# Performance work log

Measured on AMD Instinct MI355X. Metric: run time of the kernel, lower is better.

The kernel has to match this reference:

```python
import jax, jax.numpy as jnp
import numpy as np

N = 100000
E = 3200000
IN_C = 256
HID = 64
OUT_C = 2
EPS = 1e-5


def setup_inputs() -> dict:
    key = jax.random.key(0)
    ks = jax.random.split(key, 8)
    x = jax.random.normal(ks[0], (N, IN_C), dtype=jnp.float32)
    edge_index = jax.random.randint(ks[1], (2, E), 0, N, dtype=jnp.int64)
    # GCNConv weights (PyG: out = A_hat @ (x W) + b)
    W1 = jax.random.normal(ks[2], (IN_C, HID), dtype=jnp.float32) / np.sqrt(IN_C)
    b1 = jnp.zeros((HID,), dtype=jnp.float32)
    W2 = jax.random.normal(ks[3], (HID, OUT_C), dtype=jnp.float32) / np.sqrt(HID)
    b2 = jnp.zeros((OUT_C,), dtype=jnp.float32)
    # BatchNorm affine params
    g1 = jnp.ones((HID,), dtype=jnp.float32)
    be1 = jnp.zeros((HID,), dtype=jnp.float32)
    g2 = jnp.ones((OUT_C,), dtype=jnp.float32)
    be2 = jnp.zeros((OUT_C,), dtype=jnp.float32)
    # Decoder linear
    Wd = jax.random.normal(ks[4], (OUT_C, IN_C), dtype=jnp.float32) / np.sqrt(OUT_C)
    bd = jnp.zeros((IN_C,), dtype=jnp.float32)
    return {"x": x, "edge_index": edge_index, "W1": W1, "b1": b1, "g1": g1,
            "be1": be1, "W2": W2, "b2": b2, "g2": g2, "be2": be2,
            "Wd": Wd, "bd": bd}


def gcn_conv(x, W, b, src, dst, n):
    # x: [N, Cin] -> [N, Cout]; symmetric-normalized aggregation with self-loops
    xw = x @ W  # [N, Cout]
    loops = jnp.arange(n, dtype=src.dtype)
    s = jnp.concatenate([src, loops])  # [E+N]
    d = jnp.concatenate([dst, loops])
    deg = jax.ops.segment_sum(jnp.ones_like(d, dtype=x.dtype), d, num_segments=n)
    dinv = jax.lax.rsqrt(deg)  # deg >= 1 thanks to self-loops
    norm = dinv[s] * dinv[d]   # [E+N]
    out = jax.ops.segment_sum(norm[:, None] * xw[s], d, num_segments=n)
    return out + b


def batch_norm(x, gamma, beta):
    # training-mode BN over node dim, biased variance (torch semantics)
    mu = jnp.mean(x, axis=0)
    var = jnp.mean(jnp.square(x - mu), axis=0)
    return (x - mu) * jax.lax.rsqrt(var + EPS) * gamma + beta


def reference(x, edge_index, W1, b1, g1, be1, W2, b2, g2, be2, Wd, bd):
    src, dst = edge_index[0], edge_index[1]
    n = x.shape[0]
    h = gcn_conv(x, W1, b1, src, dst, n)
    h = jax.nn.relu(batch_norm(h, g1, be1))
    # dropout: identity (inference)
    z = batch_norm(gcn_conv(h, W2, b2, src, dst, n), g2, be2)
    return z @ Wd + bd  # decoder: [N, IN_C]
```

## Files before the change

### kernel.cpp

```cpp
#include <hip/hip_runtime.h>
#include <hip/hip_bf16.h>

#define NN 100000
#define NE 3200000
#define INC 256
#define HID 64
#define OUTC 2
#define EPSV 1e-5f

#define NBUCK 128
#define BCAP  26000
#define BIN_CHUNK 4096
#define BIN_K 16
#define BIN_GRID ((NE + BIN_CHUNK - 1) / BIN_CHUNK)

#define NQUART 25000

typedef short short8 __attribute__((ext_vector_type(8)));
typedef float f32x4 __attribute__((ext_vector_type(4)));

static __device__ __forceinline__ float bf2f(unsigned short u) {
    return __uint_as_float((unsigned)u << 16);
}
static __device__ __forceinline__ unsigned short f2bf(float f) {
    __hip_bfloat16 hb = __float2bfloat16(f);
    return *(unsigned short*)&hb;
}

__global__ __launch_bounds__(256) void bin_kernel(const int* __restrict__ src,
                                                  const int* __restrict__ dst,
                                                  int* __restrict__ gtail,
                                                  unsigned int* __restrict__ pbuf) {
    __shared__ int bcnt[NBUCK], bbase[NBUCK];
    int t = threadIdx.x;
    if (t < NBUCK) bcnt[t] = 0;
    __syncthreads();
    int base = blockIdx.x * BIN_CHUNK;
    int s[BIN_K], d[BIN_K], sl[BIN_K], bk[BIN_K];
#pragma unroll
    for (int r = 0; r < BIN_K; r++) {
        int i = base + r * 256 + t;
        bool v = i < NE;
        s[r] = v ? src[i] : 0;
        d[r] = v ? dst[i] : 0;
        bk[r] = (int)(((unsigned)d[r] * (unsigned)NBUCK) / (unsigned)NN);
        sl[r] = v ? atomicAdd(&bcnt[bk[r]], 1) : 0;
    }
    __syncthreads();
    if (t < NBUCK) bbase[t] = bcnt[t] ? atomicAdd(&gtail[t], bcnt[t]) : 0;
    __syncthreads();
#pragma unroll
    for (int r = 0; r < BIN_K; r++) {
        int i = base + r * 256 + t;
        if (i < NE) {
            int b = bk[r];
            int nbase = (b * NN + NBUCK - 1) >> 7;
            pbuf[(size_t)b * BCAP + bbase[b] + sl[r]] =
                ((unsigned)(d[r] - nbase) << 17) | (unsigned)s[r];
        }
    }
}

__global__ void bscan_kernel(const int* __restrict__ gtail, int* __restrict__ bbase) {
    __shared__ int wtot[2];
    int t = threadIdx.x;
    int lane = t & 63, wave = t >> 6;
    int v = gtail[t];
    int s = v;
    for (int o = 1; o < 64; o <<= 1) {
        int u = __shfl_up(s, o);
        if (lane >= o) s += u;
    }
    if (lane == 63) wtot[wave] = s;
    __syncthreads();
    int add = (wave == 1) ? wtot[0] : 0;
    bbase[t] = s - v + add;
}

__global__ __launch_bounds__(256) void build_kernel(const unsigned int* __restrict__ pbuf,
                                                    const int* __restrict__ gtail,
                                                    const int* __restrict__ bbase,
                                                    int* __restrict__ rowptr,
                                                    float* __restrict__ dinv,
                                                    int* __restrict__ e_src) {
    __shared__ int h[800], rp[800];
    __shared__ int wsum[4];
    int b = blockIdx.x, t = threadIdx.x;
    int nb = (b * NN + NBUCK - 1) >> 7;
    int ne_ = ((b + 1) * NN + NBUCK - 1) >> 7;
    int range = ne_ - nb;
    for (int i = t; i < range; i += 256) h[i] = 0;
    __syncthreads();
    int ecnt = gtail[b];
    const unsigned int* p = pbuf + (size_t)b * BCAP;
    for (int i = t; i < ecnt; i += 256) atomicAdd(&h[p[i] >> 17], 1);
    __syncthreads();
    int idx = t * 4;
    int c0 = (idx + 0 < range) ? h[idx + 0] : 0;
    int c1 = (idx + 1 < range) ? h[idx + 1] : 0;
    int c2 = (idx + 2 < range) ? h[idx + 2] : 0;
    int c3 = (idx + 3 < range) ? h[idx + 3] : 0;
    int local = c0 + c1 + c2 + c3;
    int lane = t & 63, wave = t >> 6;
    int s = local;
    for (int o = 1; o < 64; o <<= 1) {
        int u = __shfl_up(s, o);
        if (lane >= o) s += u;
    }
    if (lane == 63) wsum[wave] = s;
    __syncthreads();
    if (t == 0) {
        int run = 0;
        for (int w = 0; w < 4; w++) { int x = wsum[w]; wsum[w] = run; run += x; }
    }
    __syncthreads();
    int start = wsum[wave] + (s - local);
    int gb = bbase[b];
    if (idx + 0 < range) { rp[idx + 0] = start;                rowptr[nb + idx + 0] = gb + start;                dinv[nb + idx + 0] = rsqrtf((float)(c0 + 1)); }
    if (idx + 1 < range) { rp[idx + 1] = start + c0;           rowptr[nb + idx + 1] = gb + start + c0;           dinv[nb + idx + 1] = rsqrtf((float)(c1 + 1)); }
    if (idx + 2 < range) { rp[idx + 2] = start + c0 + c1;      rowptr[nb + idx + 2] = gb + start + c0 + c1;      dinv[nb + idx + 2] = rsqrtf((float)(c2 + 1)); }
    if (idx + 3 < range) { rp[idx + 3] = start + c0 + c1 + c2; rowptr[nb + idx + 3] = gb + start + c0 + c1 + c2; dinv[nb + idx + 3] = rsqrtf((float)(c3 + 1)); }
    if (b == NBUCK - 1 && t == 0) rowptr[NN] = NE;
    __syncthreads();
    for (int i = t; i < range; i += 256) h[i] = 0;
    __syncthreads();
    for (int i = t; i < ecnt; i += 256) {
        unsigned int k = p[i];
        int loc = k >> 17;
        int pos = gb + rp[loc] + atomicAdd(&h[loc], 1);
        e_src[pos] = (int)(k & 0x1FFFFu);
    }
}

__global__ __launch_bounds__(256) void wprep_kernel(const float* __restrict__ W1,
                                                    unsigned short* __restrict__ Wtb) {
    int t = blockIdx.x * 256 + threadIdx.x;
    int c = t & 63;
    int k = t >> 6;
    Wtb[c * 256 + k] = f2bf(W1[k * 64 + c]);
}

#define G1_ROWS 32
#define LDP 264
__global__ __launch_bounds__(256) void gemm1_kernel(const float* __restrict__ x,
                                                    const unsigned short* __restrict__ Wtb,
                                                    const float* __restrict__ dinv,
                                                    unsigned short* __restrict__ xw1h) {
    __shared__ unsigned short xt[G1_ROWS * LDP];
    __shared__ unsigned short wt[HID * LDP];
    int t = threadIdx.x;
    size_t base = (size_t)blockIdx.x * G1_ROWS;

    const float4* xg = (const float4*)(x + base * INC);
#pragma unroll
    for (int ii = 0; ii < 8; ii++) {
        int idx4 = ii * 256 + t;
        float4 v = xg[idx4];
        int f = idx4 * 4;
        int row = f >> 8, k = f & 255;
        ushort4 u;
        u.x = f2bf(v.x); u.y = f2bf(v.y); u.z = f2bf(v.z); u.w = f2bf(v.w);
        *(ushort4*)(xt + row * LDP + k) = u;
    }
    const int4* wsrc = (const int4*)Wtb;
#pragma unroll
    for (int ii = 0; ii < 8; ii++) {
        int idx4 = ii * 256 + t;
        int4 v = wsrc[idx4];
        int e16 = idx4 * 8;
        int c = e16 >> 8, k = e16 & 255;
        *(int4*)(wt + c * LDP + k) = v;
    }
    __syncthreads();

    int lane = t & 63;
    int wave = t >> 6;
    int l15 = lane & 15;
    int hi = lane >> 4;
    int rgrp = wave & 1;
    int cgrp = wave >> 1;
    const unsigned short* ap = xt + (rgrp * 16 + l15) * LDP;
    const unsigned short* bp0 = wt + (cgrp * 32 + l15) * LDP;
    const unsigned short* bp1 = bp0 + 16 * LDP;
    f32x4 acc0 = {0.f, 0.f, 0.f, 0.f};
    f32x4 acc1 = {0.f, 0.f, 0.f, 0.f};
#pragma unroll
    for (int kk = 0; kk < 8; kk++) {
        int ko = kk * 32 + hi * 8;
        short8 a  = *(const short8*)(ap + ko);
        short8 b0 = *(const short8*)(bp0 + ko);
        short8 b1 = *(const short8*)(bp1 + ko);
        acc0 = __builtin_amdgcn_mfma_f32_16x16x32_bf16(a, b0, acc0, 0, 0, 0);
        acc1 = __builtin_amdgcn_mfma_f32_16x16x32_bf16(a, b1, acc1, 0, 0, 0);
    }
    unsigned short* ph = xw1h + (size_t)cgrp * NN * 32;
#pragma unroll
    for (int i = 0; i < 4; i++) {
        int grow = (int)base + rgrp * 16 + hi * 4 + i;
        float dv = dinv[grow];
        ph[(size_t)grow * 32 + l15]      = f2bf(acc0[i] * dv);
        ph[(size_t)grow * 32 + l15 + 16] = f2bf(acc1[i] * dv);
    }
}

__global__ __launch_bounds__(256) void agg1_kernel(const unsigned short* __restrict__ xw1h,
                                                   const int* __restrict__ rowptr,
                                                   const int* __restrict__ e_src,
                                                   const float* __restrict__ dinv,
                                                   const float* __restrict__ b1,
                                                   float* __restrict__ h1h,
                                                   float* __restrict__ sums1) {
    __shared__ float lsum[4][32], lsq[4][32];
    int t = threadIdx.x;
    int lane = t & 63;
    int wave = t >> 6;
    int grp = lane >> 3;
    int cl = lane & 7;
    int cohort = blockIdx.x & 7;
    int h = cohort & 1;
    int dq = cohort >> 1;
    const ushort4* plane = (const ushort4*)(xw1h + (size_t)h * NN * 32);
    float* hp = h1h + (size_t)h * NN * 32;
    float bb0 = b1[h * 32 + cl * 4 + 0];
    float bb1 = b1[h * 32 + cl * 4 + 1];
    float bb2 = b1[h * 32 + cl * 4 + 2];
    float bb3 = b1[h * 32 + cl * 4 + 3];
    int gid = ((blockIdx.x >> 3) * 4 + wave) * 8 + grp;
    int dlo = dq * NQUART;
    float ss0 = 0.f, ss1 = 0.f, ss2 = 0.f, ss3 = 0.f;
    float sq0 = 0.f, sq1 = 0.f, sq2 = 0.f, sq3 = 0.f;
    for (int d = dlo + gid; d < dlo + NQUART; d += 8192) {
        int beg = rowptr[d], end = rowptr[d + 1];
        float a0 = 0.f, a1 = 0.f, a2 = 0.f, a3 = 0.f;
        int e = beg;
        for (; e + 3 < end; e += 4) {
            int s0 = e_src[e], s1 = e_src[e + 1], s2 = e_src[e + 2], s3 = e_src[e + 3];
            ushort4 u0 = plane[(size_t)s0 * 8 + cl];
            ushort4 u1 = plane[(size_t)s1 * 8 + cl];
            ushort4 u2 = plane[(size_t)s2 * 8 + cl];
            ushort4 u3 = plane[(size_t)s3 * 8 + cl];
            a0 += bf2f(u0.x) + bf2f(u1.x) + bf2f(u2.x) + bf2f(u3.x);
            a1 += bf2f(u0.y) + bf2f(u1.y) + bf2f(u2.y) + bf2f(u3.y);
            a2 += bf2f(u0.z) + bf2f(u1.z) + bf2f(u2.z) + bf2f(u3.z);
            a3 += bf2f(u0.w) + bf2f(u1.w) + bf2f(u2.w) + bf2f(u3.w);
        }
        for (; e < end; e++) {
            int s = e_src[e];
            ushort4 u = plane[(size_t)s * 8 + cl];
            a0 += bf2f(u.x); a1 += bf2f(u.y); a2 += bf2f(u.z); a3 += bf2f(u.w);
        }
        ushort4 us = plane[(size_t)d * 8 + cl];
        a0 += bf2f(us.x); a1 += bf2f(us.y); a2 += bf2f(us.z); a3 += bf2f(us.w);
        float dv = dinv[d];
        float h0 = a0 * dv + bb0;
        float h1v = a1 * dv + bb1;
        float h2 = a2 * dv + bb2;
        float h3 = a3 * dv + bb3;
        f32x4 hv = {h0, h1v, h2, h3};
        *(f32x4*)(hp + (size_t)d * 32 + cl * 4) = hv;
        ss0 += h0; sq0 += h0 * h0;
        ss1 += h1v; sq1 += h1v * h1v;
        ss2 += h2; sq2 += h2 * h2;
        ss3 += h3; sq3 += h3 * h3;
    }
#pragma unroll
    for (int o = 8; o < 64; o <<= 1) {
        ss0 += __shfl_xor(ss0, o); sq0 += __shfl_xor(sq0, o);
        ss1 += __shfl_xor(ss1, o); sq1 += __shfl_xor(sq1, o);
        ss2 += __shfl_xor(ss2, o); sq2 += __shfl_xor(sq2, o);
        ss3 += __shfl_xor(ss3, o); sq3 += __shfl_xor(sq3, o);
    }
    if (grp == 0) {
        lsum[wave][cl * 4 + 0] = ss0; lsq[wave][cl * 4 + 0] = sq0;
        lsum[wave][cl * 4 + 1] = ss1; lsq[wave][cl * 4 + 1] = sq1;
        lsum[wave][cl * 4 + 2] = ss2; lsq[wave][cl * 4 + 2] = sq2;
        lsum[wave][cl * 4 + 3] = ss3; lsq[wave][cl * 4 + 3] = sq3;
    }
    __syncthreads();
    if (t < 32) {
        float S = lsum[0][t] + lsum[1][t] + lsum[2][t] + lsum[3][t];
        float Q = lsq[0][t] + lsq[1][t] + lsq[2][t] + lsq[3][t];
        atomicAdd(&sums1[h * 32 + t], S);
        atomicAdd(&sums1[64 + h * 32 + t], Q);
    }
}

__global__ __launch_bounds__(256) void gemm2_kernel(const float* __restrict__ h1h,
                                                    const float* __restrict__ sums1,
                                                    const float* __restrict__ g1,
                                                    const float* __restrict__ be1,
                                                    const float* __restrict__ W2,
                                                    const float* __restrict__ dinv,
                                                    float* __restrict__ xw2) {
    int lane = threadIdx.x & 63;
    int row = blockIdx.x * 4 + (threadIdx.x >> 6);
    if (row >= NN) return;
    int c = lane;
    const float invn = 1.0f / (float)NN;
    float mu = sums1[c] * invn;
    float var = sums1[64 + c] * invn - mu * mu;
    float sc = g1[c] * rsqrtf(var + EPSV);
    float sh = be1[c] - mu * sc;
    float hv = h1h[(size_t)(c >> 5) * NN * 32 + (size_t)row * 32 + (c & 31)] * sc + sh;
    hv = fmaxf(hv, 0.f);
    float p0 = hv * W2[c * 2 + 0];
    float p1 = hv * W2[c * 2 + 1];
    for (int o = 32; o; o >>= 1) {
        p0 += __shfl_xor(p0, o);
        p1 += __shfl_xor(p1, o);
    }
    if (lane == 0) {
        float dv = dinv[row];
        xw2[(size_t)row * 2 + 0] = p0 * dv;
        xw2[(size_t)row * 2 + 1] = p1 * dv;
    }
}

__global__ __launch_bounds__(256) void agg2_kernel(const float* __restrict__ xw2,
                                                   const int* __restrict__ rowptr,
                                                   const int* __restrict__ e_src,
                                                   const float* __restrict__ dinv,
                                                   const float* __restrict__ b2,
                                                   float* __restrict__ z2,
                                                   float* __restrict__ sums2) {
    __shared__ float red[4][4];
    int t = threadIdx.x;
    int lane = t & 63;
    int wave = t >> 6;
    int gl = lane & 7;
    int d = blockIdx.x * 32 + (t >> 3);
    int beg = rowptr[d], end = rowptr[d + 1];
    float a0 = 0.f, a1 = 0.f;
    int e = beg + gl;
    for (; e + 24 < end; e += 32) {
        int s0 = e_src[e], s1 = e_src[e + 8], s2 = e_src[e + 16], s3 = e_src[e + 24];
        float2 v0 = *(const float2*)(xw2 + (size_t)s0 * 2);
        float2 v1 = *(const float2*)(xw2 + (size_t)s1 * 2);
        float2 v2 = *(const float2*)(xw2 + (size_t)s2 * 2);
        float2 v3 = *(const float2*)(xw2 + (size_t)s3 * 2);
        a0 += v0.x + v1.x + v2.x + v3.x;
        a1 += v0.y + v1.y + v2.y + v3.y;
    }
    for (; e < end; e += 8) {
        int s = e_src[e];
        float2 v = *(const float2*)(xw2 + (size_t)s * 2);
        a0 += v.x;
        a1 += v.y;
    }
    if (gl == 0) {
        float2 sf = *(const float2*)(xw2 + (size_t)d * 2);
        a0 += sf.x;
        a1 += sf.y;
    }
    a0 += __shfl_xor(a0, 1); a1 += __shfl_xor(a1, 1);
    a0 += __shfl_xor(a0, 2); a1 += __shfl_xor(a1, 2);
    a0 += __shfl_xor(a0, 4); a1 += __shfl_xor(a1, 4);
    float dv = dinv[d];
    float z0 = a0 * dv + b2[0];
    float z1 = a1 * dv + b2[1];
    if (gl == 0) *(float2*)(z2 + (size_t)d * 2) = make_float2(z0, z1);
    float s0 = (gl == 0) ? z0 : 0.f;
    float s1 = (gl == 0) ? z1 : 0.f;
    float q0 = (gl == 0) ? z0 * z0 : 0.f;
    float q1 = (gl == 0) ? z1 * z1 : 0.f;
    for (int o = 8; o < 64; o <<= 1) {
        s0 += __shfl_xor(s0, o); s1 += __shfl_xor(s1, o);
        q0 += __shfl_xor(q0, o); q1 += __shfl_xor(q1, o);
    }
    if (lane == 0) { red[wave][0] = s0; red[wave][1] = s1; red[wave][2] = q0; red[wave][3] = q1; }
    __syncthreads();
    if (t < 4) {
        float v = red[0][t] + red[1][t] + red[2][t] + red[3][t];
        atomicAdd(&sums2[(blockIdx.x & 7) * 4 + t], v);
    }
}

__global__ __launch_bounds__(256) void decoder_kernel(const float* __restrict__ z2,
                                                      const float* __restrict__ sums2,
                                                      const float* __restrict__ g2,
                                                      const float* __restrict__ be2,
                                                      const float* __restrict__ Wd,
                                                      const float* __restrict__ bd,
                                                      float* __restrict__ out) {
    int g = blockIdx.x * 256 + threadIdx.x;
    int row = g >> 6;
    int c4 = (g & 63) * 4;
    float t0 = 0.f, t1 = 0.f, t2 = 0.f, t3 = 0.f;
#pragma unroll
    for (int bk = 0; bk < 8; bk++) {
        t0 += sums2[bk * 4 + 0]; t1 += sums2[bk * 4 + 1];
        t2 += sums2[bk * 4 + 2]; t3 += sums2[bk * 4 + 3];
    }
    const float invn = 1.0f / (float)NN;
    float mu0 = t0 * invn, mu1 = t1 * invn;
    float v0 = t2 * invn - mu0 * mu0;
    float v1 = t3 * invn - mu1 * mu1;
    float sc0 = g2[0] * rsqrtf(v0 + EPSV), sh0 = be2[0] - mu0 * sc0;
    float sc1 = g2[1] * rsqrtf(v1 + EPSV), sh1 = be2[1] - mu1 * sc1;
    float zb0 = z2[(size_t)row * 2 + 0] * sc0 + sh0;
    float zb1 = z2[(size_t)row * 2 + 1] * sc1 + sh1;
    float4 w0 = *(const float4*)(Wd + c4);
    float4 w1 = *(const float4*)(Wd + INC + c4);
    float4 bb = *(const float4*)(bd + c4);
    float4 o;
    o.x = zb0 * w0.x + zb1 * w1.x + bb.x;
    o.y = zb0 * w0.y + zb1 * w1.y + bb.y;
    o.z = zb0 * w0.z + zb1 * w1.z + bb.z;
    o.w = zb0 * w0.w + zb1 * w1.w + bb.w;
    *(float4*)(out + (size_t)row * INC + c4) = o;
}

static inline size_t align256(size_t x) { return (x + 255) & ~(size_t)255; }

extern "C" void kernel_launch(void* const* d_in, const int* in_sizes, int n_in,
                              void* d_out, int out_size, void* d_ws, size_t ws_size,
                              hipStream_t stream) {
    const float* x  = (const float*)d_in[0];
    const int*   ei = (const int*)d_in[1];
    const float* W1 = (const float*)d_in[2];
    const float* b1 = (const float*)d_in[3];
    const float* g1 = (const float*)d_in[4];
    const float* be1 = (const float*)d_in[5];
    const float* W2 = (const float*)d_in[6];
    const float* b2 = (const float*)d_in[7];
    const float* g2 = (const float*)d_in[8];
    const float* be2 = (const float*)d_in[9];
    const float* Wd = (const float*)d_in[10];
    const float* bd = (const float*)d_in[11];
    float* out = (float*)d_out;

    const int* src = ei;
    const int* dst = ei + NE;

    char* ws = (char*)d_ws;
    size_t off = 0;
    int* gtail = (int*)(ws + off);      off = align256(off + NBUCK * 4);
    float* sums1 = (float*)(ws + off);  off = align256(off + 128 * 4);
    float* sums2 = (float*)(ws + off);  off = align256(off + 32 * 4);
    size_t zero_bytes = off;
    int* bbase = (int*)(ws + off);      off = align256(off + NBUCK * 4);
    int* rowptr = (int*)(ws + off);     off = align256(off + (NN + 1) * 4);
    float* dinv = (float*)(ws + off);   off = align256(off + NN * 4);
    unsigned short* Wtb = (unsigned short*)(ws + off); off = align256(off + (size_t)HID * INC * 2);
    unsigned int* pbuf = (unsigned int*)(ws + off); off = align256(off + (size_t)NBUCK * BCAP * 4 + 4096);
    int* e_src = (int*)(ws + off);      off = align256(off + (size_t)NE * 4 + 64);
    unsigned short* xw1h = (unsigned short*)(ws + off); off = align256(off + (size_t)NN * HID * 2);
    float* h1h = (float*)(ws + off);    off = align256(off + (size_t)NN * HID * 4);
    float* xw2 = (float*)(ws + off);    off = align256(off + (size_t)NN * 2 * 4);
    float* z2 = (float*)(ws + off);     off = align256(off + (size_t)NN * 2 * 4);
    (void)ws_size; (void)in_sizes; (void)n_in; (void)out_size;

    hipMemsetAsync(d_ws, 0, zero_bytes, stream);

    bin_kernel<<<BIN_GRID, 256, 0, stream>>>(src, dst, gtail, pbuf);
    bscan_kernel<<<1, 128, 0, stream>>>(gtail, bbase);
    build_kernel<<<NBUCK, 256, 0, stream>>>(pbuf, gtail, bbase, rowptr, dinv, e_src);
    wprep_kernel<<<64, 256, 0, stream>>>(W1, Wtb);
    gemm1_kernel<<<NN / G1_ROWS, 256, 0, stream>>>(x, Wtb, dinv, xw1h);
    agg1_kernel<<<2048, 256, 0, stream>>>(xw1h, rowptr, e_src, dinv, b1, h1h, sums1);
    gemm2_kernel<<<(NN + 3) / 4, 256, 0, stream>>>(h1h, sums1, g1, be1, W2, dinv, xw2);
    agg2_kernel<<<NN * 8 / 256, 256, 0, stream>>>(xw2, rowptr, e_src, dinv, b2, z2, sums2);
    decoder_kernel<<<(NN * HID) / 256, 256, 0, stream>>>(z2, sums2, g2, be2, Wd, bd, out);
}
```

Baseline: 292.5 us.

## Load GEMM1 A-operand directly from global memory, each wave computing all 64 columns

The first GEMM no longer stages the fp32 x tile into LDS as bf16. Each lane now reads its x row straight from global memory, converts it to bf16 in registers and feeds the MFMA. Each wave now computes 16 rows across all 64 output columns, and the block tile grows to 64 rows, so W is staged in LDS once per 64 rows. This removes the LDS write/read round trip and one barrier for x, at the cost of per-lane strided global loads (each lane reads 32 bytes per k-step from a different row) and bounds checks for the partial last block.

```diff
diff --git a/kernel.cpp b/kernel.cpp
--- a/kernel.cpp
+++ b/kernel.cpp
@@ -140,28 +140,16 @@
     Wtb[c * 256 + k] = f2bf(W1[k * 64 + c]);
 }
 
-#define G1_ROWS 32
+#define G1_ROWS 64
 #define LDP 264
 __global__ __launch_bounds__(256) void gemm1_kernel(const float* __restrict__ x,
                                                     const unsigned short* __restrict__ Wtb,
                                                     const float* __restrict__ dinv,
                                                     unsigned short* __restrict__ xw1h) {
-    __shared__ unsigned short xt[G1_ROWS * LDP];
     __shared__ unsigned short wt[HID * LDP];
     int t = threadIdx.x;
     size_t base = (size_t)blockIdx.x * G1_ROWS;
 
-    const float4* xg = (const float4*)(x + base * INC);
-#pragma unroll
-    for (int ii = 0; ii < 8; ii++) {
-        int idx4 = ii * 256 + t;
-        float4 v = xg[idx4];
-        int f = idx4 * 4;
-        int row = f >> 8, k = f & 255;
-        ushort4 u;
-        u.x = f2bf(v.x); u.y = f2bf(v.y); u.z = f2bf(v.z); u.w = f2bf(v.w);
-        *(ushort4*)(xt + row * LDP + k) = u;
-    }
     const int4* wsrc = (const int4*)Wtb;
 #pragma unroll
     for (int ii = 0; ii < 8; ii++) {
@@ -177,29 +165,47 @@
     int wave = t >> 6;
     int l15 = lane & 15;
     int hi = lane >> 4;
-    int rgrp = wave & 1;
-    int cgrp = wave >> 1;
-    const unsigned short* ap = xt + (rgrp * 16 + l15) * LDP;
-    const unsigned short* bp0 = wt + (cgrp * 32 + l15) * LDP;
+    int row = (int)base + wave * 16 + l15;
+    const float* xr = x + (size_t)(row < NN ? row : 0) * INC;
+    const unsigned short* bp0 = wt + l15 * LDP;
     const unsigned short* bp1 = bp0 + 16 * LDP;
+    const unsigned short* bp2 = bp0 + 32 * LDP;
+    const unsigned short* bp3 = bp0 + 48 * LDP;
     f32x4 acc0 = {0.f, 0.f, 0.f, 0.f};
     f32x4 acc1 = {0.f, 0.f, 0.f, 0.f};
+    f32x4 acc2 = {0.f, 0.f, 0.f, 0.f};
+    f32x4 acc3 = {0.f, 0.f, 0.f, 0.f};
 #pragma unroll
     for (int kk = 0; kk < 8; kk++) {
         int ko = kk * 32 + hi * 8;
-        short8 a  = *(const short8*)(ap + ko);
+        float4 xa = *(const float4*)(xr + ko);
+        float4 xb = *(const float4*)(xr + ko + 4);
+        short8 a;
+        a[0] = (short)f2bf(xa.x); a[1] = (short)f2bf(xa.y);
+        a[2] = (short)f2bf(xa.z); a[3] = (short)f2bf(xa.w);
+        a[4] = (short)f2bf(xb.x); a[5] = (short)f2bf(xb.y);
+        a[6] = (short)f2bf(xb.z); a[7] = (short)f2bf(xb.w);
         short8 b0 = *(const short8*)(bp0 + ko);
         short8 b1 = *(const short8*)(bp1 + ko);
+        short8 b2 = *(const short8*)(bp2 + ko);
+        short8 b3 = *(const short8*)(bp3 + ko);
         acc0 = __builtin_amdgcn_mfma_f32_16x16x32_bf16(a, b0, acc0, 0, 0, 0);
         acc1 = __builtin_amdgcn_mfma_f32_16x16x32_bf16(a, b1, acc1, 0, 0, 0);
-    }
-    unsigned short* ph = xw1h + (size_t)cgrp * NN * 32;
+        acc2 = __builtin_amdgcn_mfma_f32_16x16x32_bf16(a, b2, acc2, 0, 0, 0);
+        acc3 = __builtin_amdgcn_mfma_f32_16x16x32_bf16(a, b3, acc3, 0, 0, 0);
+    }
+    unsigned short* ph0 = xw1h;
+    unsigned short* ph1 = xw1h + (size_t)NN * 32;
 #pragma unroll
     for (int i = 0; i < 4; i++) {
-        int grow = (int)base + rgrp * 16 + hi * 4 + i;
-        float dv = dinv[grow];
-        ph[(size_t)grow * 32 + l15]      = f2bf(acc0[i] * dv);
-        ph[(size_t)grow * 32 + l15 + 16] = f2bf(acc1[i] * dv);
+        int grow = (int)base + wave * 16 + hi * 4 + i;
+        if (grow < NN) {
+            float dv = dinv[grow];
+            ph0[(size_t)grow * 32 + l15]      = f2bf(acc0[i] * dv);
+            ph0[(size_t)grow * 32 + l15 + 16] = f2bf(acc1[i] * dv);
+            ph1[(size_t)grow * 32 + l15]      = f2bf(acc2[i] * dv);
+            ph1[(size_t)grow * 32 + l15 + 16] = f2bf(acc3[i] * dv);
+        }
     }
 }
 
@@ -456,7 +462,7 @@
     bscan_kernel<<<1, 128, 0, stream>>>(gtail, bbase);
     build_kernel<<<NBUCK, 256, 0, stream>>>(pbuf, gtail, bbase, rowptr, dinv, e_src);
     wprep_kernel<<<64, 256, 0, stream>>>(W1, Wtb);
-    gemm1_kernel<<<NN / G1_ROWS, 256, 0, stream>>>(x, Wtb, dinv, xw1h);
+    gemm1_kernel<<<(NN + G1_ROWS - 1) / G1_ROWS, 256, 0, stream>>>(x, Wtb, dinv, xw1h);
     agg1_kernel<<<2048, 256, 0, stream>>>(xw1h, rowptr, e_src, dinv, b1, h1h, sums1);
     gemm2_kernel<<<(NN + 3) / 4, 256, 0, stream>>>(h1h, sums1, g1, be1, W2, dinv, xw2);
     agg2_kernel<<<NN * 8 / 256, 256, 0, stream>>>(xw2, rowptr, e_src, dinv, b2, z2, sums2);
```

Result: no change. 293.6 us (+0.4%).

## Split layer-1 gather by source-node half to shrink the random-access working set

Applied to the files above, without the earlier changes.

In the CSR build, each destination's edge list is ordered so that sources below 50000 come first, and the count of those edges is stored per node. The layer-1 features are stored as four planes (source half × channel half). The gather then runs as two passes, each touching only one half of the source features, so the randomly accessed working set is smaller and fits better in cache. The cost is an extra launch, a write and re-read of partial sums through h1h, and extra shared atomics in the build. The separate bucket-scan kernel is folded into the build kernel.

```diff
diff --git a/kernel.cpp b/kernel.cpp
--- a/kernel.cpp
+++ b/kernel.cpp
@@ -15,6 +15,7 @@
 #define BIN_GRID ((NE + BIN_CHUNK - 1) / BIN_CHUNK)
 
 #define NQUART 25000
+#define SHALF 50000
 
 typedef short short8 __attribute__((ext_vector_type(8)));
 typedef float f32x4 __attribute__((ext_vector_type(4)));
@@ -61,47 +62,51 @@
     }
 }
 
-__global__ void bscan_kernel(const int* __restrict__ gtail, int* __restrict__ bbase) {
-    __shared__ int wtot[2];
-    int t = threadIdx.x;
-    int lane = t & 63, wave = t >> 6;
-    int v = gtail[t];
-    int s = v;
-    for (int o = 1; o < 64; o <<= 1) {
-        int u = __shfl_up(s, o);
-        if (lane >= o) s += u;
-    }
-    if (lane == 63) wtot[wave] = s;
-    __syncthreads();
-    int add = (wave == 1) ? wtot[0] : 0;
-    bbase[t] = s - v + add;
-}
-
 __global__ __launch_bounds__(256) void build_kernel(const unsigned int* __restrict__ pbuf,
                                                     const int* __restrict__ gtail,
-                                                    const int* __restrict__ bbase,
                                                     int* __restrict__ rowptr,
+                                                    int* __restrict__ cnt0,
                                                     float* __restrict__ dinv,
                                                     int* __restrict__ e_src) {
-    __shared__ int h[800], rp[800];
-    __shared__ int wsum[4];
+    __shared__ int hS[800], h0S[800], rpS[800], f1S[800];
+    __shared__ int wsum[4], wtot2[2], lbb[NBUCK];
     int b = blockIdx.x, t = threadIdx.x;
+    int lane = t & 63, wave = t >> 6;
+    int bv = 0, bs = 0;
+    if (t < NBUCK) {
+        bv = gtail[t];
+        bs = bv;
+        for (int o = 1; o < 64; o <<= 1) {
+            int u = __shfl_up(bs, o);
+            if (lane >= o) bs += u;
+        }
+        if (lane == 63) wtot2[wave] = bs;
+    }
+    __syncthreads();
+    if (t < NBUCK) lbb[t] = bs - bv + ((t >= 64) ? wtot2[0] : 0);
+    __syncthreads();
+    int gb = lbb[b];
+
     int nb = (b * NN + NBUCK - 1) >> 7;
     int ne_ = ((b + 1) * NN + NBUCK - 1) >> 7;
     int range = ne_ - nb;
-    for (int i = t; i < range; i += 256) h[i] = 0;
+    for (int i = t; i < range; i += 256) { hS[i] = 0; h0S[i] = 0; }
     __syncthreads();
     int ecnt = gtail[b];
     const unsigned int* p = pbuf + (size_t)b * BCAP;
-    for (int i = t; i < ecnt; i += 256) atomicAdd(&h[p[i] >> 17], 1);
+    for (int i = t; i < ecnt; i += 256) {
+        unsigned int k = p[i];
+        int loc = k >> 17;
+        atomicAdd(&hS[loc], 1);
+        if ((k & 0x1FFFFu) < SHALF) atomicAdd(&h0S[loc], 1);
+    }
     __syncthreads();
     int idx = t * 4;
-    int c0 = (idx + 0 < range) ? h[idx + 0] : 0;
-    int c1 = (idx + 1 < range) ? h[idx + 1] : 0;
-    int c2 = (idx + 2 < range) ? h[idx + 2] : 0;
-    int c3 = (idx + 3 < range) ? h[idx + 3] : 0;
+    int c0 = (idx + 0 < range) ? hS[idx + 0] : 0;
+    int c1 = (idx + 1 < range) ? hS[idx + 1] : 0;
+    int c2 = (idx + 2 < range) ? hS[idx + 2] : 0;
+    int c3 = (idx + 3 < range) ? hS[idx + 3] : 0;
     int local = c0 + c1 + c2 + c3;
-    int lane = t & 63, wave = t >> 6;
     int s = local;
     for (int o = 1; o < 64; o <<= 1) {
         int u = __shfl_up(s, o);
@@ -115,20 +120,22 @@
     }
     __syncthreads();
     int start = wsum[wave] + (s - local);
-    int gb = bbase[b];
-    if (idx + 0 < range) { rp[idx + 0] = start;                rowptr[nb + idx + 0] = gb + start;                dinv[nb + idx + 0] = rsqrtf((float)(c0 + 1)); }
-    if (idx + 1 < range) { rp[idx + 1] = start + c0;           rowptr[nb + idx + 1] = gb + start + c0;           dinv[nb + idx + 1] = rsqrtf((float)(c1 + 1)); }
-    if (idx + 2 < range) { rp[idx + 2] = start + c0 + c1;      rowptr[nb + idx + 2] = gb + start + c0 + c1;      dinv[nb + idx + 2] = rsqrtf((float)(c2 + 1)); }
-    if (idx + 3 < range) { rp[idx + 3] = start + c0 + c1 + c2; rowptr[nb + idx + 3] = gb + start + c0 + c1 + c2; dinv[nb + idx + 3] = rsqrtf((float)(c3 + 1)); }
+    if (idx + 0 < range) { rpS[idx + 0] = start;                rowptr[nb + idx + 0] = gb + start;                cnt0[nb + idx + 0] = h0S[idx + 0]; dinv[nb + idx + 0] = rsqrtf((float)(c0 + 1)); }
+    if (idx + 1 < range) { rpS[idx + 1] = start + c0;           rowptr[nb + idx + 1] = gb + start + c0;           cnt0[nb + idx + 1] = h0S[idx + 1]; dinv[nb + idx + 1] = rsqrtf((float)(c1 + 1)); }
+    if (idx + 2 < range) { rpS[idx + 2] = start + c0 + c1;      rowptr[nb + idx + 2] = gb + start + c0 + c1;      cnt0[nb + idx + 2] = h0S[idx + 2]; dinv[nb + idx + 2] = rsqrtf((float)(c2 + 1)); }
+    if (idx + 3 < range) { rpS[idx + 3] = start + c0 + c1 + c2; rowptr[nb + idx + 3] = gb + start + c0 + c1 + c2; cnt0[nb + idx + 3] = h0S[idx + 3]; dinv[nb + idx + 3] = rsqrtf((float)(c3 + 1)); }
     if (b == NBUCK - 1 && t == 0) rowptr[NN] = NE;
     __syncthreads();
-    for (int i = t; i < range; i += 256) h[i] = 0;
+    for (int i = t; i < range; i += 256) { hS[i] = 0; f1S[i] = 0; }
     __syncthreads();
     for (int i = t; i < ecnt; i += 256) {
         unsigned int k = p[i];
         int loc = k >> 17;
-        int pos = gb + rp[loc] + atomicAdd(&h[loc], 1);
-        e_src[pos] = (int)(k & 0x1FFFFu);
+        int srcn = (int)(k & 0x1FFFFu);
+        int pos;
+        if (srcn < SHALF) pos = gb + rpS[loc] + atomicAdd(&hS[loc], 1);
+        else              pos = gb + rpS[loc] + h0S[loc] + atomicAdd(&f1S[loc], 1);
+        e_src[pos] = srcn;
     }
 }
 
@@ -145,7 +152,7 @@
 __global__ __launch_bounds__(256) void gemm1_kernel(const float* __restrict__ x,
                                                     const unsigned short* __restrict__ Wtb,
                                                     const float* __restrict__ dinv,
-                                                    unsigned short* __restrict__ xw1h) {
+                                                    unsigned short* __restrict__ xw1s) {
     __shared__ unsigned short xt[G1_ROWS * LDP];
     __shared__ unsigned short wt[HID * LDP];
     int t = threadIdx.x;
@@ -193,24 +200,23 @@
         acc0 = __builtin_amdgcn_mfma_f32_16x16x32_bf16(a, b0, acc0, 0, 0, 0);
         acc1 = __builtin_amdgcn_mfma_f32_16x16x32_bf16(a, b1, acc1, 0, 0, 0);
     }
-    unsigned short* ph = xw1h + (size_t)cgrp * NN * 32;
 #pragma unroll
     for (int i = 0; i < 4; i++) {
         int grow = (int)base + rgrp * 16 + hi * 4 + i;
         float dv = dinv[grow];
-        ph[(size_t)grow * 32 + l15]      = f2bf(acc0[i] * dv);
-        ph[(size_t)grow * 32 + l15 + 16] = f2bf(acc1[i] * dv);
-    }
-}
-
-__global__ __launch_bounds__(256) void agg1_kernel(const unsigned short* __restrict__ xw1h,
-                                                   const int* __restrict__ rowptr,
-                                                   const int* __restrict__ e_src,
-                                                   const float* __restrict__ dinv,
-                                                   const float* __restrict__ b1,
-                                                   float* __restrict__ h1h,
-                                                   float* __restrict__ sums1) {
-    __shared__ float lsum[4][32], lsq[4][32];
+        int sh = grow >= SHALF;
+        unsigned short* ph = xw1s + ((size_t)(sh * 2 + cgrp)) * SHALF * 32
+                                  + (size_t)(grow - sh * SHALF) * 32;
+        ph[l15]      = f2bf(acc0[i] * dv);
+        ph[l15 + 16] = f2bf(acc1[i] * dv);
+    }
+}
+
+__global__ __launch_bounds__(256) void agg1a_kernel(const unsigned short* __restrict__ xw1s,
+                                                    const int* __restrict__ rowptr,
+                                                    const int* __restrict__ cnt0,
+                                                    const int* __restrict__ e_src,
+                                                    float* __restrict__ h1h) {
     int t = threadIdx.x;
     int lane = t & 63;
     int wave = t >> 6;
@@ -219,18 +225,12 @@
     int cohort = blockIdx.x & 7;
     int h = cohort & 1;
     int dq = cohort >> 1;
-    const ushort4* plane = (const ushort4*)(xw1h + (size_t)h * NN * 32);
+    const ushort4* plane = (const ushort4*)(xw1s + (size_t)h * SHALF * 32);
     float* hp = h1h + (size_t)h * NN * 32;
-    float bb0 = b1[h * 32 + cl * 4 + 0];
-    float bb1 = b1[h * 32 + cl * 4 + 1];
-    float bb2 = b1[h * 32 + cl * 4 + 2];
-    float bb3 = b1[h * 32 + cl * 4 + 3];
     int gid = ((blockIdx.x >> 3) * 4 + wave) * 8 + grp;
     int dlo = dq * NQUART;
-    float ss0 = 0.f, ss1 = 0.f, ss2 = 0.f, ss3 = 0.f;
-    float sq0 = 0.f, sq1 = 0.f, sq2 = 0.f, sq3 = 0.f;
     for (int d = dlo + gid; d < dlo + NQUART; d += 8192) {
-        int beg = rowptr[d], end = rowptr[d + 1];
+        int beg = rowptr[d], end = beg + cnt0[d];
         float a0 = 0.f, a1 = 0.f, a2 = 0.f, a3 = 0.f;
         int e = beg;
         for (; e + 3 < end; e += 4) {
@@ -249,13 +249,68 @@
             ushort4 u = plane[(size_t)s * 8 + cl];
             a0 += bf2f(u.x); a1 += bf2f(u.y); a2 += bf2f(u.z); a3 += bf2f(u.w);
         }
-        ushort4 us = plane[(size_t)d * 8 + cl];
-        a0 += bf2f(us.x); a1 += bf2f(us.y); a2 += bf2f(us.z); a3 += bf2f(us.w);
+        f32x4 pv = {a0, a1, a2, a3};
+        *(f32x4*)(hp + (size_t)d * 32 + cl * 4) = pv;
+    }
+}
+
+__global__ __launch_bounds__(256) void agg1b_kernel(const unsigned short* __restrict__ xw1s,
+                                                    const int* __restrict__ rowptr,
+                                                    const int* __restrict__ cnt0,
+                                                    const int* __restrict__ e_src,
+                                                    const float* __restrict__ dinv,
+                                                    const float* __restrict__ b1,
+                                                    float* __restrict__ h1h,
+                                                    float* __restrict__ sums1) {
+    __shared__ float lsum[4][32], lsq[4][32];
+    int t = threadIdx.x;
+    int lane = t & 63;
+    int wave = t >> 6;
+    int grp = lane >> 3;
+    int cl = lane & 7;
+    int cohort = blockIdx.x & 7;
+    int h = cohort & 1;
+    int dq = cohort >> 1;
+    const ushort4* plane = (const ushort4*)(xw1s + (size_t)(2 + h) * SHALF * 32);
+    float* hp = h1h + (size_t)h * NN * 32;
+    float bb0 = b1[h * 32 + cl * 4 + 0];
+    float bb1 = b1[h * 32 + cl * 4 + 1];
+    float bb2 = b1[h * 32 + cl * 4 + 2];
+    float bb3 = b1[h * 32 + cl * 4 + 3];
+    int gid = ((blockIdx.x >> 3) * 4 + wave) * 8 + grp;
+    int dlo = dq * NQUART;
+    float ss0 = 0.f, ss1 = 0.f, ss2 = 0.f, ss3 = 0.f;
+    float sq0 = 0.f, sq1 = 0.f, sq2 = 0.f, sq3 = 0.f;
+    for (int d = dlo + gid; d < dlo + NQUART; d += 8192) {
+        int beg = rowptr[d] + cnt0[d], end = rowptr[d + 1];
+        float a0 = 0.f, a1 = 0.f, a2 = 0.f, a3 = 0.f;
+        int e = beg;
+        for (; e + 3 < end; e += 4) {
+            int s0 = e_src[e] - SHALF, s1 = e_src[e + 1] - SHALF;
+            int s2 = e_src[e + 2] - SHALF, s3 = e_src[e + 3] - SHALF;
+            ushort4 u0 = plane[(size_t)s0 * 8 + cl];
+            ushort4 u1 = plane[(size_t)s1 * 8 + cl];
+            ushort4 u2 = plane[(size_t)s2 * 8 + cl];
+            ushort4 u3 = plane[(size_t)s3 * 8 + cl];
+            a0 += bf2f(u0.x) + bf2f(u1.x) + bf2f(u2.x) + bf2f(u3.x);
+            a1 += bf2f(u0.y) + bf2f(u1.y) + bf2f(u2.y) + bf2f(u3.y);
+            a2 += bf2f(u0.z) + bf2f(u1.z) + bf2f(u2.z) + bf2f(u3.z);
+            a3 += bf2f(u0.w) + bf2f(u1.w) + bf2f(u2.w) + bf2f(u3.w);
+        }
+        for (; e < end; e++) {
+            int s = e_src[e] - SHALF;
+            ushort4 u = plane[(size_t)s * 8 + cl];
+            a0 += bf2f(u.x); a1 += bf2f(u.y); a2 += bf2f(u.z); a3 += bf2f(u.w);
+        }
+        f32x4 pv = *(const f32x4*)(hp + (size_t)d * 32 + cl * 4);
+        int dsh = d >= SHALF;
+        const ushort4* sp = (const ushort4*)(xw1s + (size_t)(dsh * 2 + h) * SHALF * 32);
+        ushort4 us = sp[(size_t)(d - dsh * SHALF) * 8 + cl];
         float dv = dinv[d];
-        float h0 = a0 * dv + bb0;
-        float h1v = a1 * dv + bb1;
-        float h2 = a2 * dv + bb2;
-        float h3 = a3 * dv + bb3;
+        float h0 = (pv[0] + a0 + bf2f(us.x)) * dv + bb0;
+        float h1v = (pv[1] + a1 + bf2f(us.y)) * dv + bb1;
+        float h2 = (pv[2] + a2 + bf2f(us.z)) * dv + bb2;
+        float h3 = (pv[3] + a3 + bf2f(us.w)) * dv + bb3;
         f32x4 hv = {h0, h1v, h2, h3};
         *(f32x4*)(hp + (size_t)d * 32 + cl * 4) = hv;
         ss0 += h0; sq0 += h0 * h0;
@@ -438,13 +493,13 @@
     float* sums1 = (float*)(ws + off);  off = align256(off + 128 * 4);
     float* sums2 = (float*)(ws + off);  off = align256(off + 32 * 4);
     size_t zero_bytes = off;
-    int* bbase = (int*)(ws + off);      off = align256(off + NBUCK * 4);
     int* rowptr = (int*)(ws + off);     off = align256(off + (NN + 1) * 4);
+    int* cnt0 = (int*)(ws + off);       off = align256(off + NN * 4);
     float* dinv = (float*)(ws + off);   off = align256(off + NN * 4);
     unsigned short* Wtb = (unsigned short*)(ws + off); off = align256(off + (size_t)HID * INC * 2);
     unsigned int* pbuf = (unsigned int*)(ws + off); off = align256(off + (size_t)NBUCK * BCAP * 4 + 4096);
     int* e_src = (int*)(ws + off);      off = align256(off + (size_t)NE * 4 + 64);
-    unsigned short* xw1h = (unsigned short*)(ws + off); off = align256(off + (size_t)NN * HID * 2);
+    unsigned short* xw1s = (unsigned short*)(ws + off); off = align256(off + (size_t)NN * HID * 2);
     float* h1h = (float*)(ws + off);    off = align256(off + (size_t)NN * HID * 4);
     float* xw2 = (float*)(ws + off);    off = align256(off + (size_t)NN * 2 * 4);
     float* z2 = (float*)(ws + off);     off = align256(off + (size_t)NN * 2 * 4);
@@ -453,11 +508,11 @@
     hipMemsetAsync(d_ws, 0, zero_bytes, stream);
 
     bin_kernel<<<BIN_GRID, 256, 0, stream>>>(src, dst, gtail, pbuf);
-    bscan_kernel<<<1, 128, 0, stream>>>(gtail, bbase);
-    build_kernel<<<NBUCK, 256, 0, stream>>>(pbuf, gtail, bbase, rowptr, dinv, e_src);
+    build_kernel<<<NBUCK, 256, 0, stream>>>(pbuf, gtail, rowptr, cnt0, dinv, e_src);
     wprep_kernel<<<64, 256, 0, stream>>>(W1, Wtb);
-    gemm1_kernel<<<NN / G1_ROWS, 256, 0, stream>>>(x, Wtb, dinv, xw1h);
-    agg1_kernel<<<2048, 256, 0, stream>>>(xw1h, rowptr, e_src, dinv, b1, h1h, sums1);
+    gemm1_kernel<<<NN / G1_ROWS, 256, 0, stream>>>(x, Wtb, dinv, xw1s);
+    agg1a_kernel<<<2048, 256, 0, stream>>>(xw1s, rowptr, cnt0, e_src, h1h);
+    agg1b_kernel<<<2048, 256, 0, stream>>>(xw1s, rowptr, cnt0, e_src, dinv, b1, h1h, sums1);
     gemm2_kernel<<<(NN + 3) / 4, 256, 0, stream>>>(h1h, sums1, g1, be1, W2, dinv, xw2);
     agg2_kernel<<<NN * 8 / 256, 256, 0, stream>>>(xw2, rowptr, e_src, dinv, b2, z2, sums2);
     decoder_kernel<<<(NN * HID) / 256, 256, 0, stream>>>(z2, sums2, g2, be2, Wd, bd, out);
```

New measurement: 300.2 us. 2.6% more time.
